# Performance work log

Measured on AMD Instinct MI355X. Metric: run time of the kernel, lower is better.

## Reference

```python
import jax, jax.numpy as jnp
import numpy as np

NEG_SLOPE_ATT = 0.2   # GATConv attention LeakyReLU
NEG_SLOPE_OUT = 0.01  # F.leaky_relu_ default on bend branch


def _gat(x, edge_index, edge_attr, W, a_src, a_dst, We, a_edge, bias):
    # Single-graph PyG GATConv (heads=1, concat=False, add_self_loops=True,
    # fill_value='mean' for self-loop edge_attr, dropout inactive in eval).
    # x: [N, F], edge_index: [2, E], edge_attr: [E, ED]
    N = x.shape[0]
    E = edge_attr.shape[0]
    h = x @ W  # [N, C] projected node features
    src, dst = edge_index[0], edge_index[1]
    # self-loop edge_attr = mean of incoming edge_attr per dst node
    deg = jax.ops.segment_sum(jnp.ones((E,), x.dtype), dst, num_segments=N)
    loop_attr = jax.ops.segment_sum(edge_attr, dst, num_segments=N) / jnp.maximum(deg, 1.0)[:, None]
    sl = jnp.arange(N)
    src2 = jnp.concatenate([src, sl])
    dst2 = jnp.concatenate([dst, sl])
    ea = jnp.concatenate([edge_attr, loop_attr], axis=0)  # [E+N, ED]
    eh = ea @ We  # [E+N, C]
    alpha = (h * a_src).sum(-1)[src2] + (h * a_dst).sum(-1)[dst2] + (eh * a_edge).sum(-1)
    alpha = jax.nn.leaky_relu(alpha, NEG_SLOPE_ATT)
    # per-dst-node softmax (stable)
    amax = jax.ops.segment_max(alpha, dst2, num_segments=N)
    ex = jnp.exp(alpha - amax[dst2])
    den = jax.ops.segment_sum(ex, dst2, num_segments=N)
    coef = ex / den[dst2]
    out = jax.ops.segment_sum(coef[:, None] * h[src2], dst2, num_segments=N)
    return out + bias


def setup_inputs() -> dict:
    key = jax.random.key(0)
    B, S, n, F, C, ED = 8, 16, 256, 128, 128, 4
    N = S * n
    Eb, Es = N * 16, n * 16
    ks = jax.random.split(key, 20)
    s = 0.1
    return {
        "x": jax.random.normal(ks[0], (B, S, n, F), jnp.float32),
        "section_edge_index": jax.random.randint(ks[1], (2, Es), 0, n),
        "bend_edge_index": jax.random.randint(ks[2], (2, Eb), 0, N),
        "section_edge_attr": jax.random.normal(ks[3], (B, Es, ED), jnp.float32),
        "bend_edge_attr": jax.random.normal(ks[4], (B, Eb, ED), jnp.float32),
        "enc_W": jax.random.normal(ks[5], (ED, ED), jnp.float32) * s,
        "enc_b": jnp.zeros((ED,), jnp.float32),
        "Wb": jax.random.normal(ks[6], (F, C), jnp.float32) * s,
        "a_src_b": jax.random.normal(ks[7], (C,), jnp.float32) * s,
        "a_dst_b": jax.random.normal(ks[8], (C,), jnp.float32) * s,
        "We_b": jax.random.normal(ks[9], (ED, C), jnp.float32) * s,
        "a_edge_b": jax.random.normal(ks[10], (C,), jnp.float32) * s,
        "bias_b": jnp.zeros((C,), jnp.float32),
        "Ws": jax.random.normal(ks[11], (F, C), jnp.float32) * s,
        "a_src_s": jax.random.normal(ks[12], (C,), jnp.float32) * s,
        "a_dst_s": jax.random.normal(ks[13], (C,), jnp.float32) * s,
        "We_s": jax.random.normal(ks[14], (ED, C), jnp.float32) * s,
        "a_edge_s": jax.random.normal(ks[15], (C,), jnp.float32) * s,
        "bias_s": jnp.zeros((C,), jnp.float32),
        "fuse_w": jnp.ones((2,), jnp.float32),
    }


def reference(x, section_edge_index, bend_edge_index, section_edge_attr, bend_edge_attr,
              enc_W, enc_b, Wb, a_src_b, a_dst_b, We_b, a_edge_b, bias_b,
              Ws, a_src_s, a_dst_s, We_s, a_edge_s, bias_s, fuse_w):
    B, S, n, F = x.shape
    enc_bend = bend_edge_attr @ enc_W + enc_b      # [B, Eb, ED]
    enc_sec = section_edge_attr @ enc_W + enc_b    # [B, Es, ED]
    # bend graph: one graph per batch element over all S*n nodes
    xb = x.reshape(B, S * n, F)
    gat_b = lambda xi, ei: _gat(xi, bend_edge_index, ei, Wb, a_src_b, a_dst_b, We_b, a_edge_b, bias_b)
    xb_out = jax.nn.leaky_relu(jax.vmap(gat_b)(xb, enc_bend), NEG_SLOPE_OUT)  # [B, S*n, C]
    # section graphs: one graph per (batch, section); edge_attr shared across sections
    es = jnp.broadcast_to(enc_sec[:, None], (B, S) + enc_sec.shape[1:]).reshape(B * S, *enc_sec.shape[1:])
    gat_s = lambda xi, ei: _gat(xi, section_edge_index, ei, Ws, a_src_s, a_dst_s, We_s, a_edge_s, bias_s)
    xs_out = jax.vmap(gat_s)(x.reshape(B * S, n, F), es).reshape(B, S * n, -1)
    w = jax.nn.softmax(fuse_w)
    return w[0] * xb_out + w[1] * xs_out
```

## Files before the change

### kernel.cpp

```cpp
#include <hip/hip_runtime.h>
#include <hip/hip_bf16.h>
#include <hip/hip_fp16.h>
#include <cstdint>
#include <cstddef>

#define NEG_ATT 0.2f
#define NEG_OUT 0.01f

constexpr int Bc = 8, Sc = 16, Nn = 256, Fd = 128, Cd = 128;
constexpr int NB = Sc * Nn;
constexpr int EB = NB * 16;
constexpr int ES = Nn * 16;
constexpr int NROWS = Bc * NB;
constexpr int CAP = 80;

constexpr size_t OFF_CONSTS = 0;
constexpr size_t OFF_XBF  = 4096;
constexpr size_t OFF_WTB  = OFF_XBF + (size_t)NROWS * Fd * 2;
constexpr size_t OFF_WTS  = OFF_WTB + (size_t)Fd * Cd * 2;
constexpr size_t OFF_HBP  = OFF_WTS + (size_t)Fd * Cd * 2;
constexpr size_t OFF_HSP  = OFF_HBP + (size_t)NROWS * 64 * 4;
constexpr size_t OFF_SSB  = OFF_HSP + (size_t)NROWS * 64 * 4;
constexpr size_t OFF_SDB  = OFF_SSB + (size_t)NROWS * 4;
constexpr size_t OFF_SSS  = OFF_SDB + (size_t)NROWS * 4;
constexpr size_t OFF_SDS  = OFF_SSS + (size_t)NROWS * 4;
constexpr size_t OFF_AEB  = OFF_SDS + (size_t)NROWS * 4;
constexpr size_t OFF_AES  = OFF_AEB + (size_t)Bc * EB * 4;
constexpr size_t OFF_ELLB = OFF_AES + (size_t)Bc * ES * 4;
constexpr size_t OFF_ELLS = OFF_ELLB + (size_t)NB * CAP * 4;
constexpr size_t OFF_FILB = OFF_ELLS + (size_t)Nn * CAP * 4;
constexpr size_t OFF_FILS = OFF_FILB + (size_t)NB * 4;
constexpr int ZERO_U32 = NB + Nn;


typedef short bf16x8 __attribute__((ext_vector_type(8)));
typedef float f32x4 __attribute__((ext_vector_type(4)));

__device__ inline unsigned short f2bf(float f) {
  unsigned int u = __float_as_uint(f);
  u += 0x7fffu + ((u >> 16) & 1u);
  return (unsigned short)(u >> 16);
}
__device__ inline float lrelu(float x, float s) { return x > 0.f ? x : x * s; }
__device__ inline float bflo(unsigned int u) { return __uint_as_float(u << 16); }
__device__ inline float bfhi(unsigned int u) { return __uint_as_float(u & 0xffff0000u); }
__device__ inline float wave_dot128(const float* Wrow, const float* a, int lane) {
  float2 wv = *(const float2*)(Wrow + 2 * lane);
  float2 av = *(const float2*)(a + 2 * lane);
  float p = wv.x * av.x + wv.y * av.y;
  for (int off = 32; off; off >>= 1) p += __shfl_xor(p, off);
  return p;
}
__device__ inline unsigned int pack_sc(int s, float c) {
  return ((unsigned int)s << 16) | (unsigned int)__half_as_ushort(__float2half(c));
}
__device__ inline float unpack_c(unsigned int pk) {
  return __half2float(__ushort_as_half((unsigned short)(pk & 0xffffu)));
}

__global__ __launch_bounds__(256) void k_setup(
    const float* Wb, const float* a_src_b, const float* a_dst_b,
    const float* Ws, const float* a_src_s, const float* a_dst_s,
    const float* We_b, const float* a_edge_b,
    const float* We_s, const float* a_edge_s,
    const float* fuse_w, const float* enc_W, const float* enc_b,
    float* consts, unsigned short* wtb, unsigned short* wts, unsigned int* fill_region) {
  int blk = blockIdx.x, t = threadIdx.x;
  if (blk < 128) {
    int tid = blk * 256 + t;
    int which = tid >> 14, idx = tid & 16383;
    int c = idx >> 7, k = idx & 127;
    const float* W = which ? Ws : Wb;
    unsigned short* o = which ? wts : wtb;
    o[c * 128 + k] = f2bf(W[k * 128 + c]);
  } else if (blk < 160) {
    int wave = t >> 6, lane = t & 63;
    int gw = (blk - 128) * 4 + wave;
    int base = gw * 4;
    int v = base >> 7;
    const float* W = (v < 2) ? Wb : Ws;
    const float* a = (v == 0) ? a_src_b : (v == 1) ? a_dst_b : (v == 2) ? a_src_s : a_dst_s;
#pragma unroll
    for (int k = 0; k < 4; ++k) {
      int idx = base + k, f = idx & 127;
      float p = wave_dot128(W + f * 128, a, lane);
      if (lane == 0) consts[16 + v * 128 + f] = p;
    }
  } else if (blk == 160) {
    int wave = t >> 6, lane = t & 63;
    float pb = wave_dot128(We_b + wave * 128, a_edge_b, lane);
    float ps = wave_dot128(We_s + wave * 128, a_edge_s, lane);
    if (lane == 0) { consts[2 + wave] = pb; consts[6 + wave] = ps; }
    if (t == 0) {
      float f0 = fuse_w[0], f1 = fuse_w[1];
      float m = fmaxf(f0, f1);
      float e0 = __expf(f0 - m), e1 = __expf(f1 - m);
      consts[0] = e0 / (e0 + e1);
      consts[1] = e1 / (e0 + e1);
    }
  } else if (blk == 161) {
    if (t < 16) consts[544 + t] = enc_W[t];
    else if (t < 20) consts[544 + t] = enc_b[t - 16];
  } else {
    int zid = (blk - 162) * 256 + t;
    for (int z = zid; z < ZERO_U32; z += 2 * 256) fill_region[z] = 0;
  }
}

__global__ __launch_bounds__(256) void k_front(
    const float* x, const float* consts, unsigned short* xbf,
    float* ssb, float* sdb, float* sss, float* sds,
    const int* bsrc, const int* bdst, const int* ssrcA, const int* sdst,
    int* filb, int* fils, unsigned int* ellb, unsigned int* ells,
    const float* battr, const float* sattr, float* aeb, float* aes) {
  int blk = blockIdx.x, t = threadIdx.x;
  if (blk < 8192) {
    int wid = blk * 4 + (t >> 6);
    int lane = t & 63;
    const float2 xv = *(const float2*)(x + (size_t)wid * 128 + 2 * lane);
    unsigned int pack = (unsigned int)f2bf(xv.x) | ((unsigned int)f2bf(xv.y) << 16);
    *(unsigned int*)(xbf + (size_t)wid * 128 + 2 * lane) = pack;
    const float* wa = consts + 16;
    float2 w0 = *(const float2*)(wa + 0 * 128 + 2 * lane);
    float2 w1 = *(const float2*)(wa + 1 * 128 + 2 * lane);
    float2 w2 = *(const float2*)(wa + 2 * 128 + 2 * lane);
    float2 w3 = *(const float2*)(wa + 3 * 128 + 2 * lane);
    float p0 = xv.x * w0.x + xv.y * w0.y;
    float p1 = xv.x * w1.x + xv.y * w1.y;
    float p2 = xv.x * w2.x + xv.y * w2.y;
    float p3 = xv.x * w3.x + xv.y * w3.y;
    for (int off = 32; off; off >>= 1) {
      p0 += __shfl_xor(p0, off);
      p1 += __shfl_xor(p1, off);
      p2 += __shfl_xor(p2, off);
      p3 += __shfl_xor(p3, off);
    }
    if (lane == 0) { ssb[wid] = p0; sdb[wid] = p1; sss[wid] = p2; sds[wid] = p3; }
  } else if (blk < 8192 + 272) {
    int tid = (blk - 8192) * 256 + t;
    if (tid < EB) {
      int d = bdst[tid];
      int slot = atomicAdd(&filb[d], 1);
      if (slot < CAP) ellb[(size_t)d * CAP + slot] = ((unsigned int)bsrc[tid] << 16) | (unsigned int)tid;
    } else if (tid < EB + ES) {
      int e = tid - EB;
      int d = sdst[e];
      int slot = atomicAdd(&fils[d], 1);
      if (slot < CAP) ells[(size_t)d * CAP + slot] = ((unsigned int)ssrcA[e] << 16) | (unsigned int)e;
    }
  } else {
    int idx = (blk - 8464) * 256 + t;
    const float* encW = consts + 544;
    bool isB = idx < Bc * EB;
    const float* attr = isB ? battr : sattr;
    const float* wae = consts + (isB ? 2 : 6);
    float* dst = isB ? aeb : aes;
    int id2 = isB ? idx : idx - Bc * EB;
    float4 at = *(const float4*)(attr + (size_t)id2 * 4);
    float e0 = encW[16] + at.x * encW[0] + at.y * encW[4] + at.z * encW[8]  + at.w * encW[12];
    float e1 = encW[17] + at.x * encW[1] + at.y * encW[5] + at.z * encW[9]  + at.w * encW[13];
    float e2 = encW[18] + at.x * encW[2] + at.y * encW[6] + at.z * encW[10] + at.w * encW[14];
    float e3 = encW[19] + at.x * encW[3] + at.y * encW[7] + at.z * encW[11] + at.w * encW[15];
    dst[id2] = e0 * wae[0] + e1 * wae[1] + e2 * wae[2] + e3 * wae[3];
  }
}

__global__ __launch_bounds__(256) void k_gemm2(const unsigned short* xb,
                                               const unsigned short* wtb,
                                               const unsigned short* wts,
                                               unsigned int* hbp, unsigned int* hsp) {
  int wave = threadIdx.x >> 6, lane = threadIdx.x & 63;
  int m0 = blockIdx.x * 64 + wave * 16;
  int r = lane & 15, kg = lane >> 4;
  f32x4 accB[8], accS[8];
#pragma unroll
  for (int i = 0; i < 8; ++i) { accB[i] = (f32x4){0,0,0,0}; accS[i] = (f32x4){0,0,0,0}; }
#pragma unroll
  for (int ks = 0; ks < 4; ++ks) {
    bf16x8 a = *(const bf16x8*)(xb + (size_t)(m0 + r) * 128 + ks * 32 + kg * 8);
#pragma unroll
    for (int cb = 0; cb < 8; ++cb) {
      bf16x8 bb = *(const bf16x8*)(wtb + (size_t)(cb * 16 + r) * 128 + ks * 32 + kg * 8);
      accB[cb] = __builtin_amdgcn_mfma_f32_16x16x32_bf16(a, bb, accB[cb], 0, 0, 0);
      bf16x8 bs = *(const bf16x8*)(wts + (size_t)(cb * 16 + r) * 128 + ks * 32 + kg * 8);
      accS[cb] = __builtin_amdgcn_mfma_f32_16x16x32_bf16(a, bs, accS[cb], 0, 0, 0);
    }
  }
#pragma unroll
  for (int cb = 0; cb < 4; ++cb)
#pragma unroll
    for (int i = 0; i < 4; ++i) {
      size_t idx = (size_t)(m0 + kg * 4 + i) * 64 + cb * 16 + r;
      hbp[idx] = (unsigned int)f2bf(accB[cb][i]) | ((unsigned int)f2bf(accB[cb + 4][i]) << 16);
      hsp[idx] = (unsigned int)f2bf(accS[cb][i]) | ((unsigned int)f2bf(accS[cb + 4][i]) << 16);
    }
}

__global__ __launch_bounds__(256) void k_gather(
    const float* ssb, const float* sdb, const float* aeb,
    const int* filb, const unsigned int* ellb, const unsigned int* hbp, const float* bias_b,
    const float* sss, const float* sds, const float* aes,
    const int* fils, const unsigned int* ells, const unsigned int* hsp, const float* bias_s,
    const float* consts, float* out) {
  int wg = blockIdx.x;
  int wave = threadIdx.x >> 6, lane = threadIdx.x & 63;
  int b = wg & 7;
  int i = ((wg >> 3) << 2) + wave;
  int wid = (b << 12) + i;
  int il = i & 255;
  int rowBase = wid - il;

  float oB0 = 0.f, oB1 = 0.f, oS0 = 0.f, oS1 = 0.f;

  int degB = filb[i];  if (degB > CAP) degB = CAP;
  int degS = fils[il]; if (degS > CAP) degS = CAP;
  const float* ssrcBb = ssb + ((size_t)b << 12);
  const float* ssrcGs = sss + rowBase;
  const float* aeBb = aeb + (size_t)b * EB;
  const float* aeBs = aes + (size_t)b * ES;
  const unsigned int* hBb = hbp + (((size_t)b << 12) << 6);
  const unsigned int* hGs = hsp + ((size_t)rowBase << 6);
  const unsigned int* ellBr = ellb + (size_t)i * CAP;
  const unsigned int* ellSr = ells + (size_t)il * CAP;
  unsigned int uSelfB = hbp[((size_t)wid << 6) + lane];
  unsigned int uSelfS = hsp[((size_t)wid << 6) + lane];
  float sdB = sdb[wid], sdS = sds[wid];
  float ssSelfB = ssrcBb[i], ssSelfS = ssrcGs[il];

  float mB, invB, aSB, mS, invS, aSS;

  if (degB <= 64 && degS <= 64) {
    bool vB = lane < degB, vS = lane < degS;
    unsigned int evB = vB ? ellBr[lane] : 0u;
    unsigned int evS = vS ? ellSr[lane] : 0u;
    int sB = evB >> 16, sS = evS >> 16;
    int eB = evB & 0xffffu, eS = evS & 0xffffu;
    float aevB = vB ? aeBb[eB] : 0.f;
    float aevS = vS ? aeBs[eS] : 0.f;
    float xsB = ssrcBb[sB];
    float xsS = ssrcGs[sS];

    float asumB = aevB, asumS = aevS;
    for (int off = 32; off; off >>= 1) {
      asumB += __shfl_xor(asumB, off);
      asumS += __shfl_xor(asumS, off);
    }
    aSB = lrelu(ssSelfB + sdB + asumB / (float)(degB > 0 ? degB : 1), NEG_ATT);
    aSS = lrelu(ssSelfS + sdS + asumS / (float)(degS > 0 ? degS : 1), NEG_ATT);
    float aB = vB ? lrelu(xsB + sdB + aevB, NEG_ATT) : aSB;
    float aS2 = vS ? lrelu(xsS + sdS + aevS, NEG_ATT) : aSS;
    mB = fmaxf(aB, aSB); mS = fmaxf(aS2, aSS);
    for (int off = 32; off; off >>= 1) {
      mB = fmaxf(mB, __shfl_xor(mB, off));
      mS = fmaxf(mS, __shfl_xor(mS, off));
    }
    float cB = vB ? __expf(aB - mB) : 0.f;
    float cS2 = vS ? __expf(aS2 - mS) : 0.f;
    float seB = cB, seS = cS2;
    for (int off = 32; off; off >>= 1) {
      seB += __shfl_xor(seB, off);
      seS += __shfl_xor(seS, off);
    }
    seB += __expf(aSB - mB); seS += __expf(aSS - mS);
    invB = 1.f / seB; invS = 1.f / seS;

    unsigned int pkB = pack_sc(sB, cB * invB);
    unsigned int pkS = pack_sc(sS, cS2 * invS);

    int maxD = degB > degS ? degB : degS;
    for (int j = 0; j < maxD; j += 4) {
      unsigned int ub[4], us[4]; float cb4[4], cs4[4];
#pragma unroll
      for (int t = 0; t < 4; ++t) {
        unsigned int pB = (unsigned int)__builtin_amdgcn_readlane((int)pkB, j + t);
        unsigned int pS = (unsigned int)__builtin_amdgcn_readlane((int)pkS, j + t);
        cb4[t] = unpack_c(pB);
        cs4[t] = unpack_c(pS);
        ub[t] = (hBb + ((size_t)(pB >> 16) << 6))[lane];
        us[t] = (hGs + ((size_t)(pS >> 16) << 6))[lane];
      }
#pragma unroll
      for (int t = 0; t < 4; ++t) {
        oB0 += cb4[t] * bflo(ub[t]); oB1 += cb4[t] * bfhi(ub[t]);
        oS0 += cs4[t] * bflo(us[t]); oS1 += cs4[t] * bfhi(us[t]);
      }
    }
  } else {
    {
      float asum = 0.f;
      for (int p = lane; p < degB; p += 64) asum += aeBb[ellBr[p] & 0xffffu];
      for (int off = 32; off; off >>= 1) asum += __shfl_xor(asum, off);
      aSB = lrelu(ssSelfB + sdB + asum / (float)(degB > 0 ? degB : 1), NEG_ATT);
      mB = aSB;
      for (int p = lane; p < degB; p += 64) {
        unsigned int v = ellBr[p];
        mB = fmaxf(mB, lrelu(ssrcBb[v >> 16] + sdB + aeBb[v & 0xffffu], NEG_ATT));
      }
      for (int off = 32; off; off >>= 1) mB = fmaxf(mB, __shfl_xor(mB, off));
      float se = 0.f;
      for (int p = lane; p < degB; p += 64) {
        unsigned int v = ellBr[p];
        se += __expf(lrelu(ssrcBb[v >> 16] + sdB + aeBb[v & 0xffffu], NEG_ATT) - mB);
      }
      for (int off = 32; off; off >>= 1) se += __shfl_xor(se, off);
      se += __expf(aSB - mB);
      invB = 1.f / se;
      for (int j = 0; j < degB; ++j) {
        unsigned int v = ellBr[j];
        int s = v >> 16;
        float c = __expf(lrelu(ssrcBb[s] + sdB + aeBb[v & 0xffffu], NEG_ATT) - mB) * invB;
        unsigned int u = (hBb + ((size_t)s << 6))[lane];
        oB0 += c * bflo(u); oB1 += c * bfhi(u);
      }
    }
    {
      float asum = 0.f;
      for (int p = lane; p < degS; p += 64) asum += aeBs[ellSr[p] & 0xffffu];
      for (int off = 32; off; off >>= 1) asum += __shfl_xor(asum, off);
      aSS = lrelu(ssSelfS + sdS + asum / (float)(degS > 0 ? degS : 1), NEG_ATT);
      mS = aSS;
      for (int p = lane; p < degS; p += 64) {
        unsigned int v = ellSr[p];
        mS = fmaxf(mS, lrelu(ssrcGs[v >> 16] + sdS + aeBs[v & 0xffffu], NEG_ATT));
      }
      for (int off = 32; off; off >>= 1) mS = fmaxf(mS, __shfl_xor(mS, off));
      float se = 0.f;
      for (int p = lane; p < degS; p += 64) {
        unsigned int v = ellSr[p];
        se += __expf(lrelu(ssrcGs[v >> 16] + sdS + aeBs[v & 0xffffu], NEG_ATT) - mS);
      }
      for (int off = 32; off; off >>= 1) se += __shfl_xor(se, off);
      se += __expf(aSS - mS);
      invS = 1.f / se;
      for (int j = 0; j < degS; ++j) {
        unsigned int v = ellSr[j];
        int s = v >> 16;
        float c = __expf(lrelu(ssrcGs[s] + sdS + aeBs[v & 0xffffu], NEG_ATT) - mS) * invS;
        unsigned int u = (hGs + ((size_t)s << 6))[lane];
        oS0 += c * bflo(u); oS1 += c * bfhi(u);
      }
    }
  }

  {
    float cSelfB = __expf(aSB - mB) * invB;
    oB0 += cSelfB * bflo(uSelfB); oB1 += cSelfB * bfhi(uSelfB);
    float cSelfS = __expf(aSS - mS) * invS;
    oS0 += cSelfS * bflo(uSelfS); oS1 += cSelfS * bfhi(uSelfS);
  }

  float w0 = consts[0], w1 = consts[1];
  size_t o = (size_t)wid << 7;
  out[o + lane]      = w0 * lrelu(oB0 + bias_b[lane], NEG_OUT)      + w1 * (oS0 + bias_s[lane]);
  out[o + 64 + lane] = w0 * lrelu(oB1 + bias_b[lane + 64], NEG_OUT) + w1 * (oS1 + bias_s[lane + 64]);
}

extern "C" void kernel_launch(void* const* d_in, const int* in_sizes, int n_in,
                              void* d_out, int out_size, void* d_ws, size_t ws_size,
                              hipStream_t stream) {
  (void)in_sizes; (void)n_in; (void)out_size; (void)ws_size;
  const float* x        = (const float*)d_in[0];
  const int*   sec_ei   = (const int*)d_in[1];
  const int*   bend_ei  = (const int*)d_in[2];
  const float* sec_attr = (const float*)d_in[3];
  const float* bend_attr= (const float*)d_in[4];
  const float* enc_W    = (const float*)d_in[5];
  const float* enc_b    = (const float*)d_in[6];
  const float* Wb       = (const float*)d_in[7];
  const float* a_src_b  = (const float*)d_in[8];
  const float* a_dst_b  = (const float*)d_in[9];
  const float* We_b     = (const float*)d_in[10];
  const float* a_edge_b = (const float*)d_in[11];
  const float* bias_b   = (const float*)d_in[12];
  const float* Ws       = (const float*)d_in[13];
  const float* a_src_s  = (const float*)d_in[14];
  const float* a_dst_s  = (const float*)d_in[15];
  const float* We_s     = (const float*)d_in[16];
  const float* a_edge_s = (const float*)d_in[17];
  const float* bias_s   = (const float*)d_in[18];
  const float* fuse_w   = (const float*)d_in[19];
  float* out = (float*)d_out;

  char* ws = (char*)d_ws;
  float* consts = (float*)(ws + OFF_CONSTS);
  unsigned short* xbf = (unsigned short*)(ws + OFF_XBF);
  unsigned short* wtb = (unsigned short*)(ws + OFF_WTB);
  unsigned short* wts = (unsigned short*)(ws + OFF_WTS);
  unsigned int* hbp = (unsigned int*)(ws + OFF_HBP);
  unsigned int* hsp = (unsigned int*)(ws + OFF_HSP);
  float* ssb = (float*)(ws + OFF_SSB);
  float* sdb = (float*)(ws + OFF_SDB);
  float* sss = (float*)(ws + OFF_SSS);
  float* sds = (float*)(ws + OFF_SDS);
  float* aeb = (float*)(ws + OFF_AEB);
  float* aes = (float*)(ws + OFF_AES);
  unsigned int* ellb = (unsigned int*)(ws + OFF_ELLB);
  unsigned int* ells = (unsigned int*)(ws + OFF_ELLS);
  int* filb = (int*)(ws + OFF_FILB);
  int* fils = (int*)(ws + OFF_FILS);
  unsigned int* fill_region = (unsigned int*)(ws + OFF_FILB);

  const int* bend_src = bend_ei;
  const int* bend_dst = bend_ei + EB;
  const int* sec_src  = sec_ei;
  const int* sec_dst  = sec_ei + ES;

  k_setup<<<164, 256, 0, stream>>>(Wb, a_src_b, a_dst_b, Ws, a_src_s, a_dst_s,
                                   We_b, a_edge_b, We_s, a_edge_s, fuse_w,
                                   enc_W, enc_b, consts, wtb, wts, fill_region);

  k_front<<<10640, 256, 0, stream>>>(x, consts, xbf, ssb, sdb, sss, sds,
                                     bend_src, bend_dst, sec_src, sec_dst,
                                     filb, fils, ellb, ells,
                                     bend_attr, sec_attr, aeb, aes);

  k_gemm2<<<NROWS / 64, 256, 0, stream>>>(xbf, wtb, wts, hbp, hsp);

  k_gather<<<NROWS / 4, 256, 0, stream>>>(ssb, sdb, aeb, filb, ellb, hbp, bias_b,
                                          sss, sds, aes, fils, ells, hsp, bias_s,
                                          consts, out);
}
```

Before: 80.35 us.

## Fuse bf16 conversion and score dots into GEMM; stage gather coefficients in LDS

Result: faster. 70.97 us (-11.7%).

```diff
diff --git a/kernel.cpp b/kernel.cpp
--- a/kernel.cpp
+++ b/kernel.cpp
@@ -1,6 +1,5 @@
 #include <hip/hip_runtime.h>
 #include <hip/hip_bf16.h>
-#include <hip/hip_fp16.h>
 #include <cstdint>
 #include <cstddef>
 
@@ -15,8 +14,7 @@
 constexpr int CAP = 80;
 
 constexpr size_t OFF_CONSTS = 0;
-constexpr size_t OFF_XBF  = 4096;
-constexpr size_t OFF_WTB  = OFF_XBF + (size_t)NROWS * Fd * 2;
+constexpr size_t OFF_WTB  = 4096;
 constexpr size_t OFF_WTS  = OFF_WTB + (size_t)Fd * Cd * 2;
 constexpr size_t OFF_HBP  = OFF_WTS + (size_t)Fd * Cd * 2;
 constexpr size_t OFF_HSP  = OFF_HBP + (size_t)NROWS * 64 * 4;
@@ -50,12 +48,6 @@
   float p = wv.x * av.x + wv.y * av.y;
   for (int off = 32; off; off >>= 1) p += __shfl_xor(p, off);
   return p;
-}
-__device__ inline unsigned int pack_sc(int s, float c) {
-  return ((unsigned int)s << 16) | (unsigned int)__half_as_ushort(__float2half(c));
-}
-__device__ inline float unpack_c(unsigned int pk) {
-  return __half2float(__ushort_as_half((unsigned short)(pk & 0xffffu)));
 }
 
 __global__ __launch_bounds__(256) void k_setup(
@@ -107,49 +99,77 @@
   }
 }
 
-__global__ __launch_bounds__(256) void k_front(
-    const float* x, const float* consts, unsigned short* xbf,
+constexpr int GEMM_BLKS = NROWS / 64;
+constexpr int ENC_BLKS  = (Bc * (EB + ES)) / 256;
+constexpr int SCAT_BLKS = (EB + ES + 255) / 256;
+
+__global__ __launch_bounds__(256) void k_work(
+    const float* x, const float* consts,
+    const unsigned short* wtb, const unsigned short* wts,
+    unsigned int* hbp, unsigned int* hsp,
     float* ssb, float* sdb, float* sss, float* sds,
+    const float* battr, const float* sattr, float* aeb, float* aes,
     const int* bsrc, const int* bdst, const int* ssrcA, const int* sdst,
-    int* filb, int* fils, unsigned int* ellb, unsigned int* ells,
-    const float* battr, const float* sattr, float* aeb, float* aes) {
+    int* filb, int* fils, unsigned int* ellb, unsigned int* ells) {
   int blk = blockIdx.x, t = threadIdx.x;
-  if (blk < 8192) {
-    int wid = blk * 4 + (t >> 6);
-    int lane = t & 63;
-    const float2 xv = *(const float2*)(x + (size_t)wid * 128 + 2 * lane);
-    unsigned int pack = (unsigned int)f2bf(xv.x) | ((unsigned int)f2bf(xv.y) << 16);
-    *(unsigned int*)(xbf + (size_t)wid * 128 + 2 * lane) = pack;
+  if (blk < GEMM_BLKS) {
+    int wave = t >> 6, lane = t & 63;
+    int m0 = blk * 64 + wave * 16;
+    int r = lane & 15, kg = lane >> 4;
+    f32x4 accB[8], accS[8];
+#pragma unroll
+    for (int i = 0; i < 8; ++i) { accB[i] = (f32x4){0,0,0,0}; accS[i] = (f32x4){0,0,0,0}; }
+    float p0 = 0.f, p1 = 0.f, p2 = 0.f, p3 = 0.f;
     const float* wa = consts + 16;
-    float2 w0 = *(const float2*)(wa + 0 * 128 + 2 * lane);
-    float2 w1 = *(const float2*)(wa + 1 * 128 + 2 * lane);
-    float2 w2 = *(const float2*)(wa + 2 * 128 + 2 * lane);
-    float2 w3 = *(const float2*)(wa + 3 * 128 + 2 * lane);
-    float p0 = xv.x * w0.x + xv.y * w0.y;
-    float p1 = xv.x * w1.x + xv.y * w1.y;
-    float p2 = xv.x * w2.x + xv.y * w2.y;
-    float p3 = xv.x * w3.x + xv.y * w3.y;
-    for (int off = 32; off; off >>= 1) {
-      p0 += __shfl_xor(p0, off);
-      p1 += __shfl_xor(p1, off);
-      p2 += __shfl_xor(p2, off);
-      p3 += __shfl_xor(p3, off);
-    }
-    if (lane == 0) { ssb[wid] = p0; sdb[wid] = p1; sss[wid] = p2; sds[wid] = p3; }
-  } else if (blk < 8192 + 272) {
-    int tid = (blk - 8192) * 256 + t;
-    if (tid < EB) {
-      int d = bdst[tid];
-      int slot = atomicAdd(&filb[d], 1);
-      if (slot < CAP) ellb[(size_t)d * CAP + slot] = ((unsigned int)bsrc[tid] << 16) | (unsigned int)tid;
-    } else if (tid < EB + ES) {
-      int e = tid - EB;
-      int d = sdst[e];
-      int slot = atomicAdd(&fils[d], 1);
-      if (slot < CAP) ells[(size_t)d * CAP + slot] = ((unsigned int)ssrcA[e] << 16) | (unsigned int)e;
-    }
-  } else {
-    int idx = (blk - 8464) * 256 + t;
+#pragma unroll
+    for (int ks = 0; ks < 4; ++ks) {
+      int wo = ks * 32 + kg * 8;
+      const float* xrow = x + (size_t)(m0 + r) * 128 + wo;
+      float4 xa = *(const float4*)xrow;
+      float4 xc = *(const float4*)(xrow + 4);
+      float4 w0a = *(const float4*)(wa + 0 * 128 + wo), w0b = *(const float4*)(wa + 0 * 128 + wo + 4);
+      float4 w1a = *(const float4*)(wa + 1 * 128 + wo), w1b = *(const float4*)(wa + 1 * 128 + wo + 4);
+      float4 w2a = *(const float4*)(wa + 2 * 128 + wo), w2b = *(const float4*)(wa + 2 * 128 + wo + 4);
+      float4 w3a = *(const float4*)(wa + 3 * 128 + wo), w3b = *(const float4*)(wa + 3 * 128 + wo + 4);
+      p0 += xa.x*w0a.x + xa.y*w0a.y + xa.z*w0a.z + xa.w*w0a.w
+          + xc.x*w0b.x + xc.y*w0b.y + xc.z*w0b.z + xc.w*w0b.w;
+      p1 += xa.x*w1a.x + xa.y*w1a.y + xa.z*w1a.z + xa.w*w1a.w
+          + xc.x*w1b.x + xc.y*w1b.y + xc.z*w1b.z + xc.w*w1b.w;
+      p2 += xa.x*w2a.x + xa.y*w2a.y + xa.z*w2a.z + xa.w*w2a.w
+          + xc.x*w2b.x + xc.y*w2b.y + xc.z*w2b.z + xc.w*w2b.w;
+      p3 += xa.x*w3a.x + xa.y*w3a.y + xa.z*w3a.z + xa.w*w3a.w
+          + xc.x*w3b.x + xc.y*w3b.y + xc.z*w3b.z + xc.w*w3b.w;
+      bf16x8 a;
+      a[0] = (short)f2bf(xa.x); a[1] = (short)f2bf(xa.y);
+      a[2] = (short)f2bf(xa.z); a[3] = (short)f2bf(xa.w);
+      a[4] = (short)f2bf(xc.x); a[5] = (short)f2bf(xc.y);
+      a[6] = (short)f2bf(xc.z); a[7] = (short)f2bf(xc.w);
+#pragma unroll
+      for (int cb = 0; cb < 8; ++cb) {
+        bf16x8 bb = *(const bf16x8*)(wtb + (size_t)(cb * 16 + r) * 128 + wo);
+        accB[cb] = __builtin_amdgcn_mfma_f32_16x16x32_bf16(a, bb, accB[cb], 0, 0, 0);
+        bf16x8 bs = *(const bf16x8*)(wts + (size_t)(cb * 16 + r) * 128 + wo);
+        accS[cb] = __builtin_amdgcn_mfma_f32_16x16x32_bf16(a, bs, accS[cb], 0, 0, 0);
+      }
+    }
+    p0 += __shfl_xor(p0, 16); p0 += __shfl_xor(p0, 32);
+    p1 += __shfl_xor(p1, 16); p1 += __shfl_xor(p1, 32);
+    p2 += __shfl_xor(p2, 16); p2 += __shfl_xor(p2, 32);
+    p3 += __shfl_xor(p3, 16); p3 += __shfl_xor(p3, 32);
+    if (lane < 16) {
+      int row = m0 + lane;
+      ssb[row] = p0; sdb[row] = p1; sss[row] = p2; sds[row] = p3;
+    }
+#pragma unroll
+    for (int cb = 0; cb < 4; ++cb)
+#pragma unroll
+      for (int i = 0; i < 4; ++i) {
+        size_t idx = (size_t)(m0 + kg * 4 + i) * 64 + cb * 16 + r;
+        hbp[idx] = (unsigned int)f2bf(accB[cb][i]) | ((unsigned int)f2bf(accB[cb + 4][i]) << 16);
+        hsp[idx] = (unsigned int)f2bf(accS[cb][i]) | ((unsigned int)f2bf(accS[cb + 4][i]) << 16);
+      }
+  } else if (blk < GEMM_BLKS + ENC_BLKS) {
+    int idx = (blk - GEMM_BLKS) * 256 + t;
     const float* encW = consts + 544;
     bool isB = idx < Bc * EB;
     const float* attr = isB ? battr : sattr;
@@ -162,38 +182,19 @@
     float e2 = encW[18] + at.x * encW[2] + at.y * encW[6] + at.z * encW[10] + at.w * encW[14];
     float e3 = encW[19] + at.x * encW[3] + at.y * encW[7] + at.z * encW[11] + at.w * encW[15];
     dst[id2] = e0 * wae[0] + e1 * wae[1] + e2 * wae[2] + e3 * wae[3];
+  } else {
+    int tid = (blk - GEMM_BLKS - ENC_BLKS) * 256 + t;
+    if (tid < EB) {
+      int d = bdst[tid];
+      int slot = atomicAdd(&filb[d], 1);
+      if (slot < CAP) ellb[(size_t)d * CAP + slot] = ((unsigned int)bsrc[tid] << 16) | (unsigned int)tid;
+    } else if (tid < EB + ES) {
+      int e = tid - EB;
+      int d = sdst[e];
+      int slot = atomicAdd(&fils[d], 1);
+      if (slot < CAP) ells[(size_t)d * CAP + slot] = ((unsigned int)ssrcA[e] << 16) | (unsigned int)e;
+    }
   }
-}
-
-__global__ __launch_bounds__(256) void k_gemm2(const unsigned short* xb,
-                                               const unsigned short* wtb,
-                                               const unsigned short* wts,
-                                               unsigned int* hbp, unsigned int* hsp) {
-  int wave = threadIdx.x >> 6, lane = threadIdx.x & 63;
-  int m0 = blockIdx.x * 64 + wave * 16;
-  int r = lane & 15, kg = lane >> 4;
-  f32x4 accB[8], accS[8];
-#pragma unroll
-  for (int i = 0; i < 8; ++i) { accB[i] = (f32x4){0,0,0,0}; accS[i] = (f32x4){0,0,0,0}; }
-#pragma unroll
-  for (int ks = 0; ks < 4; ++ks) {
-    bf16x8 a = *(const bf16x8*)(xb + (size_t)(m0 + r) * 128 + ks * 32 + kg * 8);
-#pragma unroll
-    for (int cb = 0; cb < 8; ++cb) {
-      bf16x8 bb = *(const bf16x8*)(wtb + (size_t)(cb * 16 + r) * 128 + ks * 32 + kg * 8);
-      accB[cb] = __builtin_amdgcn_mfma_f32_16x16x32_bf16(a, bb, accB[cb], 0, 0, 0);
-      bf16x8 bs = *(const bf16x8*)(wts + (size_t)(cb * 16 + r) * 128 + ks * 32 + kg * 8);
-      accS[cb] = __builtin_amdgcn_mfma_f32_16x16x32_bf16(a, bs, accS[cb], 0, 0, 0);
-    }
-  }
-#pragma unroll
-  for (int cb = 0; cb < 4; ++cb)
-#pragma unroll
-    for (int i = 0; i < 4; ++i) {
-      size_t idx = (size_t)(m0 + kg * 4 + i) * 64 + cb * 16 + r;
-      hbp[idx] = (unsigned int)f2bf(accB[cb][i]) | ((unsigned int)f2bf(accB[cb + 4][i]) << 16);
-      hsp[idx] = (unsigned int)f2bf(accS[cb][i]) | ((unsigned int)f2bf(accS[cb + 4][i]) << 16);
-    }
 }
 
 __global__ __launch_bounds__(256) void k_gather(
@@ -202,6 +203,7 @@
     const float* sss, const float* sds, const float* aes,
     const int* fils, const unsigned int* ells, const unsigned int* hsp, const float* bias_s,
     const float* consts, float* out) {
+  __shared__ unsigned long long lds[4][128];
   int wg = blockIdx.x;
   int wave = threadIdx.x >> 6, lane = threadIdx.x & 63;
   int b = wg & 7;
@@ -228,6 +230,7 @@
   float ssSelfB = ssrcBb[i], ssSelfS = ssrcGs[il];
 
   float mB, invB, aSB, mS, invS, aSS;
+  unsigned long long* ldsw = lds[wave];
 
   if (degB <= 64 && degS <= 64) {
     bool vB = lane < degB, vS = lane < degS;
@@ -264,26 +267,53 @@
     seB += __expf(aSB - mB); seS += __expf(aSS - mS);
     invB = 1.f / seB; invS = 1.f / seS;
 
-    unsigned int pkB = pack_sc(sB, cB * invB);
-    unsigned int pkS = pack_sc(sS, cS2 * invS);
-
-    int maxD = degB > degS ? degB : degS;
-    for (int j = 0; j < maxD; j += 4) {
-      unsigned int ub[4], us[4]; float cb4[4], cs4[4];
-#pragma unroll
-      for (int t = 0; t < 4; ++t) {
-        unsigned int pB = (unsigned int)__builtin_amdgcn_readlane((int)pkB, j + t);
-        unsigned int pS = (unsigned int)__builtin_amdgcn_readlane((int)pkS, j + t);
-        cb4[t] = unpack_c(pB);
-        cs4[t] = unpack_c(pS);
-        ub[t] = (hBb + ((size_t)(pB >> 16) << 6))[lane];
-        us[t] = (hGs + ((size_t)(pS >> 16) << 6))[lane];
-      }
-#pragma unroll
-      for (int t = 0; t < 4; ++t) {
-        oB0 += cb4[t] * bflo(ub[t]); oB1 += cb4[t] * bfhi(ub[t]);
-        oS0 += cs4[t] * bflo(us[t]); oS1 += cs4[t] * bfhi(us[t]);
-      }
+    unsigned int offB = (unsigned int)sB << 8;
+    unsigned int offS = (unsigned int)sS << 8;
+    ldsw[lane]      = ((unsigned long long)__float_as_uint(cB * invB) << 32) | offB;
+    ldsw[64 + lane] = ((unsigned long long)__float_as_uint(cS2 * invS) << 32) | offS;
+
+    const char* hBc = (const char*)hBb;
+    const char* hGc = (const char*)hGs;
+    int lb4 = lane * 4;
+    int j = 0;
+    for (; j + 4 <= degB; j += 4) {
+      unsigned long long v0 = ldsw[j], v1 = ldsw[j+1], v2 = ldsw[j+2], v3 = ldsw[j+3];
+      unsigned int u0 = *(const unsigned int*)(hBc + (unsigned int)v0 + lb4);
+      unsigned int u1 = *(const unsigned int*)(hBc + (unsigned int)v1 + lb4);
+      unsigned int u2 = *(const unsigned int*)(hBc + (unsigned int)v2 + lb4);
+      unsigned int u3 = *(const unsigned int*)(hBc + (unsigned int)v3 + lb4);
+      float c0 = __uint_as_float((unsigned int)(v0 >> 32));
+      float c1 = __uint_as_float((unsigned int)(v1 >> 32));
+      float c2 = __uint_as_float((unsigned int)(v2 >> 32));
+      float c3 = __uint_as_float((unsigned int)(v3 >> 32));
+      oB0 += c0 * bflo(u0) + c1 * bflo(u1) + c2 * bflo(u2) + c3 * bflo(u3);
+      oB1 += c0 * bfhi(u0) + c1 * bfhi(u1) + c2 * bfhi(u2) + c3 * bfhi(u3);
+    }
+    for (; j < degB; ++j) {
+      unsigned long long v = ldsw[j];
+      unsigned int u = *(const unsigned int*)(hBc + (unsigned int)v + lb4);
+      float c = __uint_as_float((unsigned int)(v >> 32));
+      oB0 += c * bflo(u); oB1 += c * bfhi(u);
+    }
+    j = 0;
+    for (; j + 4 <= degS; j += 4) {
+      unsigned long long v0 = ldsw[64+j], v1 = ldsw[64+j+1], v2 = ldsw[64+j+2], v3 = ldsw[64+j+3];
+      unsigned int u0 = *(const unsigned int*)(hGc + (unsigned int)v0 + lb4);
+      unsigned int u1 = *(const unsigned int*)(hGc + (unsigned int)v1 + lb4);
+      unsigned int u2 = *(const unsigned int*)(hGc + (unsigned int)v2 + lb4);
+      unsigned int u3 = *(const unsigned int*)(hGc + (unsigned int)v3 + lb4);
+      float c0 = __uint_as_float((unsigned int)(v0 >> 32));
+      float c1 = __uint_as_float((unsigned int)(v1 >> 32));
+      float c2 = __uint_as_float((unsigned int)(v2 >> 32));
+      float c3 = __uint_as_float((unsigned int)(v3 >> 32));
+      oS0 += c0 * bflo(u0) + c1 * bflo(u1) + c2 * bflo(u2) + c3 * bflo(u3);
+      oS1 += c0 * bfhi(u0) + c1 * bfhi(u1) + c2 * bfhi(u2) + c3 * bfhi(u3);
+    }
+    for (; j < degS; ++j) {
+      unsigned long long v = ldsw[64+j];
+      unsigned int u = *(const unsigned int*)(hGc + (unsigned int)v + lb4);
+      float c = __uint_as_float((unsigned int)(v >> 32));
+      oS0 += c * bflo(u); oS1 += c * bfhi(u);
     }
   } else {
     {
@@ -383,7 +413,6 @@
 
   char* ws = (char*)d_ws;
   float* consts = (float*)(ws + OFF_CONSTS);
-  unsigned short* xbf = (unsigned short*)(ws + OFF_XBF);
   unsigned short* wtb = (unsigned short*)(ws + OFF_WTB);
   unsigned short* wts = (unsigned short*)(ws + OFF_WTS);
   unsigned int* hbp = (unsigned int*)(ws + OFF_HBP);
@@ -409,12 +438,11 @@
                                    We_b, a_edge_b, We_s, a_edge_s, fuse_w,
                                    enc_W, enc_b, consts, wtb, wts, fill_region);
 
-  k_front<<<10640, 256, 0, stream>>>(x, consts, xbf, ssb, sdb, sss, sds,
-                                     bend_src, bend_dst, sec_src, sec_dst,
-                                     filb, fils, ellb, ells,
-                                     bend_attr, sec_attr, aeb, aes);
-
-  k_gemm2<<<NROWS / 64, 256, 0, stream>>>(xbf, wtb, wts, hbp, hsp);
+  k_work<<<GEMM_BLKS + ENC_BLKS + SCAT_BLKS, 256, 0, stream>>>(
+      x, consts, wtb, wts, hbp, hsp, ssb, sdb, sss, sds,
+      bend_attr, sec_attr, aeb, aes,
+      bend_src, bend_dst, sec_src, sec_dst,
+      filb, fils, ellb, ells);
 
   k_gather<<<NROWS / 4, 256, 0, stream>>>(ssb, sdb, aeb, filb, ellb, hbp, bias_b,
                                           sss, sds, aes, fils, ells, hsp, bias_s,
```
